# Performance work log

Measured on AMD Instinct MI355X. Metric: run time of the kernel, lower is better.

The kernel has to match this reference:

```python
import jax, jax.numpy as jnp
import numpy as np

NUM_EXPERTS = 8
TOPK = 2
INPUT_DIM = 2048
OUTPUT_DIM = 2048


def setup_inputs() -> dict:
    key = jax.random.key(0)
    k_x, k_w, k_gw, k_gb = jax.random.split(key, 4)
    x = jax.random.normal(k_x, (8192, INPUT_DIM), dtype=jnp.float32)
    # experts: Linear(input_dim, output_dim*num_experts), xavier_uniform weight, zero bias
    fan_out = OUTPUT_DIM * NUM_EXPERTS
    limit = float(np.sqrt(6.0 / (INPUT_DIM + fan_out)))
    expert_w = jax.random.uniform(k_w, (fan_out, INPUT_DIM), minval=-limit, maxval=limit, dtype=jnp.float32)
    expert_b = jnp.zeros((fan_out,), dtype=jnp.float32)
    # gate: Linear(input_dim, num_experts), default torch init (uniform +-1/sqrt(fan_in))
    gl = 1.0 / float(np.sqrt(INPUT_DIM))
    gate_w = jax.random.uniform(k_gw, (NUM_EXPERTS, INPUT_DIM), minval=-gl, maxval=gl, dtype=jnp.float32)
    gate_b = jax.random.uniform(k_gb, (NUM_EXPERTS,), minval=-gl, maxval=gl, dtype=jnp.float32)
    return {"x": x, "expert_w": expert_w, "expert_b": expert_b, "gate_w": gate_w, "gate_b": gate_b}


def reference(x, expert_w, expert_b, gate_w, gate_b):
    B = x.shape[0]
    # gating
    gate_logits = x @ gate_w.T + gate_b                      # [B, E]
    gate_probs = jax.nn.softmax(gate_logits, axis=-1)
    top_k_probs, top_k_idx = jax.lax.top_k(gate_probs, TOPK)  # [B, K]
    # dense expert GEMM: all experts computed
    expert_out = x @ expert_w.T + expert_b                   # [B, E*D_out]
    expert_out = expert_out.reshape(B, NUM_EXPERTS, OUTPUT_DIM)
    # gather selected experts per token and combine
    sel = jnp.take_along_axis(expert_out, top_k_idx[:, :, None], axis=1)  # [B, K, D_out]
    out = jnp.sum(sel * top_k_probs[:, :, None], axis=1)     # [B, D_out]
    return out
```

## Files before the change

kernel.cpp:

```cpp
#include <hip/hip_runtime.h>

#define NUM_TOKENS 8192
#define DIM 2048
#define NE 8
#define BM 256
#define BN 256
#define BK 64
#define KTILES (DIM / BK)

typedef __bf16 bf16x8 __attribute__((ext_vector_type(8)));
typedef float f32x4 __attribute__((ext_vector_type(4)));

typedef __attribute__((address_space(1))) const void* as1_cvp;
typedef __attribute__((address_space(3))) void* as3_vp;

__device__ __forceinline__ unsigned short f2bf(float f) {
  unsigned int u = __float_as_uint(f);
  unsigned int lsb = (u >> 16) & 1u;
  u += 0x7fffu + lsb;
  return (unsigned short)(u >> 16);
}
__device__ __forceinline__ float bflo(unsigned int u) {
  return __uint_as_float(u << 16);
}
__device__ __forceinline__ float bfhi(unsigned int u) {
  return __uint_as_float(u & 0xffff0000u);
}

#define CFENCE() asm volatile("" ::: "memory")

__global__ __launch_bounds__(256) void convert_w_kernel(
    const float4* __restrict__ w, ushort4* __restrict__ wb) {
  int i = blockIdx.x * 256 + threadIdx.x;
  float4 v = w[i];
  ushort4 o;
  o.x = f2bf(v.x); o.y = f2bf(v.y); o.z = f2bf(v.z); o.w = f2bf(v.w);
  wb[i] = o;
}

__global__ __launch_bounds__(256) void gating_kernel(
    const float* __restrict__ x, const float* __restrict__ gw,
    const float* __restrict__ gb, unsigned short* __restrict__ xb,
    float* __restrict__ probs, int* __restrict__ routed) {
  const int wave = threadIdx.x >> 6;
  const int lane = threadIdx.x & 63;
  const int t = blockIdx.x * 4 + wave;
  const float4* xrow = (const float4*)(x + (size_t)t * DIM);
  ushort4* xbrow = (ushort4*)(xb + (size_t)t * DIM);
  float acc[NE];
#pragma unroll
  for (int e = 0; e < NE; ++e) acc[e] = 0.f;
#pragma unroll
  for (int it = 0; it < DIM / (4 * 64); ++it) {
    const int k4 = it * 64 + lane;
    float4 xv = xrow[k4];
    ushort4 o;
    o.x = f2bf(xv.x); o.y = f2bf(xv.y); o.z = f2bf(xv.z); o.w = f2bf(xv.w);
    xbrow[k4] = o;
#pragma unroll
    for (int e = 0; e < NE; ++e) {
      float4 wv = ((const float4*)(gw + (size_t)e * DIM))[k4];
      acc[e] += xv.x * wv.x + xv.y * wv.y + xv.z * wv.z + xv.w * wv.w;
    }
  }
#pragma unroll
  for (int e = 0; e < NE; ++e) {
#pragma unroll
    for (int off = 32; off > 0; off >>= 1)
      acc[e] += __shfl_xor(acc[e], off, 64);
  }
  if (lane == 0) {
    float p[NE];
    float mx = -1e30f;
#pragma unroll
    for (int e = 0; e < NE; ++e) {
      p[e] = acc[e] + gb[e];
      mx = fmaxf(mx, p[e]);
    }
    float s = 0.f;
#pragma unroll
    for (int e = 0; e < NE; ++e) { p[e] = __expf(p[e] - mx); s += p[e]; }
    float inv = 1.f / s;
#pragma unroll
    for (int e = 0; e < NE; ++e) p[e] *= inv;
    int e0 = 0;
#pragma unroll
    for (int e = 1; e < NE; ++e) if (p[e] > p[e0]) e0 = e;
    int e1 = (e0 == 0) ? 1 : 0;
#pragma unroll
    for (int e = 0; e < NE; ++e) if (e != e0 && p[e] > p[e1]) e1 = e;
    probs[t * 2 + 0] = p[e0];
    probs[t * 2 + 1] = p[e1];
    routed[t] = e0 | (e1 << 8);
  }
}

__global__ __launch_bounds__(256) void build_lists_kernel(
    const int* __restrict__ routed, int* __restrict__ lists,
    int* __restrict__ counts, int* __restrict__ tokpos) {
  const int e = blockIdx.x;
  const int tid = threadIdx.x;
  __shared__ int sc[256];
  __shared__ int sb[256];
  const int base_t = tid * (NUM_TOKENS / 256);
  int c = 0, cb = 0;
#pragma unroll 4
  for (int j = 0; j < NUM_TOKENS / 256; ++j) {
    int r = routed[base_t + j];
    int a0 = r & 0xff, a1 = (r >> 8) & 0xff;
    c += (a0 == e) + (a1 == e);
    cb += (a0 < e) + (a1 < e);
  }
  sc[tid] = c;
  sb[tid] = cb;
  __syncthreads();
  for (int ofs = 1; ofs < 256; ofs <<= 1) {
    int v = (tid >= ofs) ? sc[tid - ofs] : 0;
    int w = (tid >= ofs) ? sb[tid - ofs] : 0;
    __syncthreads();
    sc[tid] += v;
    sb[tid] += w;
    __syncthreads();
  }
  const int ebase = sb[255];
  int pos = sc[tid] - c;
#pragma unroll 4
  for (int j = 0; j < NUM_TOKENS / 256; ++j) {
    int t = base_t + j;
    int r = routed[t];
    if ((r & 0xff) == e) {
      lists[e * NUM_TOKENS + pos] = t;
      tokpos[2 * t] = ebase + pos;
      pos++;
    }
    if (((r >> 8) & 0xff) == e) {
      lists[e * NUM_TOKENS + pos] = t | 0x10000;
      tokpos[2 * t + 1] = ebase + pos;
      pos++;
    }
  }
  if (tid == 255) {
    counts[e] = sc[255];
    counts[8 + e] = ebase;
  }
}

__global__ __launch_bounds__(512, 2) void moe_gemm_kernel(
    const unsigned short* __restrict__ xb,
    const unsigned short* __restrict__ wb,
    const float* __restrict__ eb,
    const float* __restrict__ probs,
    const int* __restrict__ lists,
    const int* __restrict__ counts,
    unsigned short* __restrict__ y,
    float* __restrict__ out,
    int use_y) {
  const int e = blockIdx.z;
  const int cnt = counts[e];
  const int m0 = blockIdx.y * BM;
  if (m0 >= cnt) return;
  const int n0 = blockIdx.x * BN;

  __shared__ __attribute__((aligned(16))) unsigned short As[2][BM * BK];
  __shared__ __attribute__((aligned(16))) unsigned short Bs[2][BN * BK];

  const int tid = threadIdx.x;
  const int w = tid >> 6;
  const int ln = tid & 63;
  const int sr8 = ln >> 3;
  const int sgc = ((ln & 7) ^ sr8) * 8;

  const unsigned short* asrc[4];
  const unsigned short* bsrc[4];
#pragma unroll
  for (int rb = 0; rb < 4; ++rb) {
    int r = m0 + rb * 64 + w * 8 + sr8;
    int rc = r < cnt ? r : cnt - 1;
    int tok = lists[e * NUM_TOKENS + rc] & 0xFFFF;
    asrc[rb] = xb + (size_t)tok * DIM + sgc;
    int wr = e * DIM + n0 + rb * 64 + w * 8 + sr8;
    bsrc[rb] = wb + (size_t)wr * DIM + sgc;
  }

#define STAGE_A(buf, rb, k0)                                      \
  __builtin_amdgcn_global_load_lds(                               \
      (as1_cvp)(asrc[rb] + (k0)),                                 \
      (as3_vp)(&As[buf][((rb)*64 + w * 8) * 64]), 16, 0, 0)
#define STAGE_B(buf, rb, k0)                                      \
  __builtin_amdgcn_global_load_lds(                               \
      (as1_cvp)(bsrc[rb] + (k0)),                                 \
      (as3_vp)(&Bs[buf][((rb)*64 + w * 8) * 64]), 16, 0, 0)

#define BAR()            \
  do {                   \
    CFENCE();            \
    __builtin_amdgcn_s_barrier(); \
    CFENCE();            \
  } while (0)

  const f32x4 zero = {0.f, 0.f, 0.f, 0.f};
  f32x4 acc[8][4];
#pragma unroll
  for (int a = 0; a < 8; ++a)
#pragma unroll
    for (int b = 0; b < 4; ++b) acc[a][b] = zero;

  const int wm = w >> 2;
  const int wn = w & 3;
  const int frow = ln & 15;
  const int csel = ln >> 4;
  const int f7 = frow & 7;
  const int aro = (wm * 128 + frow) * 64;
  const int bro = (wn * 64 + frow) * 64;
  const int k0off = (csel ^ f7) * 8;
  const int k1off = ((4 + csel) ^ f7) * 8;

#pragma unroll
  for (int rb = 0; rb < 4; ++rb) STAGE_A(0, rb, 0);
#pragma unroll
  for (int rb = 0; rb < 4; ++rb) STAGE_B(0, rb, 0);

  for (int t = 0; t < KTILES; ++t) {
    const int p = t & 1;
    const int kn = (t + 1) * BK;
    if (t + 1 < KTILES) {
#pragma unroll
      for (int rb = 0; rb < 4; ++rb) STAGE_A(p ^ 1, rb, kn);
      asm volatile("s_waitcnt vmcnt(4)" ::: "memory");
    } else {
      asm volatile("s_waitcnt vmcnt(0)" ::: "memory");
    }
    BAR();
    const unsigned short* Ap = As[p];
    const unsigned short* Bp = Bs[p];
    bf16x8 af[4], bf[4];
#pragma unroll
    for (int i = 0; i < 4; ++i) {
      af[i] = *(const bf16x8*)(Ap + aro + i * 1024 + k0off);
      bf[i] = *(const bf16x8*)(Bp + bro + i * 1024 + k0off);
    }
    __builtin_amdgcn_s_setprio(1);
#pragma unroll
    for (int im = 0; im < 4; ++im)
#pragma unroll
      for (int in_ = 0; in_ < 4; ++in_)
        acc[im][in_] = __builtin_amdgcn_mfma_f32_16x16x32_bf16(
            af[im], bf[in_], acc[im][in_], 0, 0, 0);
    __builtin_amdgcn_s_setprio(0);
    BAR();
#pragma unroll
    for (int i = 0; i < 4; ++i)
      af[i] = *(const bf16x8*)(Ap + aro + (i + 4) * 1024 + k0off);
    if (t + 1 < KTILES) {
#pragma unroll
      for (int rb = 0; rb < 4; ++rb) STAGE_B(p ^ 1, rb, kn);
    }
    __builtin_amdgcn_s_setprio(1);
#pragma unroll
    for (int im = 0; im < 4; ++im)
#pragma unroll
      for (int in_ = 0; in_ < 4; ++in_)
        acc[im + 4][in_] = __builtin_amdgcn_mfma_f32_16x16x32_bf16(
            af[im], bf[in_], acc[im + 4][in_], 0, 0, 0);
    __builtin_amdgcn_s_setprio(0);
    BAR();
#pragma unroll
    for (int i = 0; i < 4; ++i) {
      af[i] = *(const bf16x8*)(Ap + aro + i * 1024 + k1off);
      bf[i] = *(const bf16x8*)(Bp + bro + i * 1024 + k1off);
    }
    __builtin_amdgcn_s_setprio(1);
#pragma unroll
    for (int im = 0; im < 4; ++im)
#pragma unroll
      for (int in_ = 0; in_ < 4; ++in_)
        acc[im][in_] = __builtin_amdgcn_mfma_f32_16x16x32_bf16(
            af[im], bf[in_], acc[im][in_], 0, 0, 0);
    __builtin_amdgcn_s_setprio(0);
    BAR();
#pragma unroll
    for (int i = 0; i < 4; ++i)
      af[i] = *(const bf16x8*)(Ap + aro + (i + 4) * 1024 + k1off);
    __builtin_amdgcn_s_setprio(1);
#pragma unroll
    for (int im = 0; im < 4; ++im)
#pragma unroll
      for (int in_ = 0; in_ < 4; ++in_)
        acc[im + 4][in_] = __builtin_amdgcn_mfma_f32_16x16x32_bf16(
            af[im], bf[in_], acc[im + 4][in_], 0, 0, 0);
    __builtin_amdgcn_s_setprio(0);
    BAR();
  }
#undef STAGE_A
#undef STAGE_B
#undef BAR

  const int quad = ln >> 4;
  const int col = ln & 15;
  const int ybase = counts[8 + e];
#pragma unroll
  for (int im = 0; im < 8; ++im) {
#pragma unroll
    for (int reg = 0; reg < 4; ++reg) {
      int r = m0 + wm * 128 + im * 16 + quad * 4 + reg;
      if (r >= cnt) continue;
      if (use_y) {
        unsigned short* yrow = y + (size_t)(ybase + r) * DIM;
#pragma unroll
        for (int in_ = 0; in_ < 4; ++in_) {
          int n = n0 + wn * 64 + in_ * 16 + col;
          yrow[n] = f2bf(acc[im][in_][reg] + eb[e * DIM + n]);
        }
      } else {
        int entry = lists[e * NUM_TOKENS + r];
        int tok = entry & 0xFFFF;
        int slot = entry >> 16;
        float pw = probs[tok * 2 + slot];
        float* orow = out + (size_t)tok * DIM;
#pragma unroll
        for (int in_ = 0; in_ < 4; ++in_) {
          int n = n0 + wn * 64 + in_ * 16 + col;
          float v = acc[im][in_][reg] + eb[e * DIM + n];
          atomicAdd(orow + n, pw * v);
        }
      }
    }
  }
}

__global__ __launch_bounds__(256) void combine_kernel(
    const unsigned short* __restrict__ y, const float* __restrict__ probs,
    const int* __restrict__ tokpos, float* __restrict__ out) {
  const int t = blockIdx.x;
  const int tid = threadIdx.x;
  const int i0 = tokpos[2 * t], i1 = tokpos[2 * t + 1];
  const float p0 = probs[2 * t], p1 = probs[2 * t + 1];
  uint4 a = ((const uint4*)(y + (size_t)i0 * DIM))[tid];
  uint4 b = ((const uint4*)(y + (size_t)i1 * DIM))[tid];
  float4 o0, o1;
  o0.x = p0 * bflo(a.x) + p1 * bflo(b.x);
  o0.y = p0 * bfhi(a.x) + p1 * bfhi(b.x);
  o0.z = p0 * bflo(a.y) + p1 * bflo(b.y);
  o0.w = p0 * bfhi(a.y) + p1 * bfhi(b.y);
  o1.x = p0 * bflo(a.z) + p1 * bflo(b.z);
  o1.y = p0 * bfhi(a.z) + p1 * bfhi(b.z);
  o1.z = p0 * bflo(a.w) + p1 * bflo(b.w);
  o1.w = p0 * bfhi(a.w) + p1 * bfhi(b.w);
  float4* orow = (float4*)(out + (size_t)t * DIM);
  orow[2 * tid] = o0;
  orow[2 * tid + 1] = o1;
}

extern "C" void kernel_launch(void* const* d_in, const int* in_sizes, int n_in,
                              void* d_out, int out_size, void* d_ws, size_t ws_size,
                              hipStream_t stream) {
  const float* x  = (const float*)d_in[0];
  const float* ew = (const float*)d_in[1];
  const float* eb = (const float*)d_in[2];
  const float* gw = (const float*)d_in[3];
  const float* gb = (const float*)d_in[4];
  float* out = (float*)d_out;
  char* p = (char*)d_ws;

  const size_t NEED = 67108864ull + 33554432ull + 67108864ull + 65536ull +
                      262144ull + 64ull + 32768ull + 65536ull;
  const int use_y = (ws_size >= NEED) ? 1 : 0;

  unsigned short* wb = (unsigned short*)p; p += 67108864;
  unsigned short* xb = (unsigned short*)p; p += 33554432;
  unsigned short* y = nullptr;
  if (use_y) { y = (unsigned short*)p; p += 67108864; }
  float* probs = (float*)p; p += 65536;
  int* lists   = (int*)p;   p += 262144;
  int* counts  = (int*)p;   p += 64;
  int* routed  = (int*)p;   p += 32768;
  int* tokpos  = (int*)p;   p += 65536;

  if (!use_y)
    hipMemsetAsync(out, 0, (size_t)NUM_TOKENS * DIM * sizeof(float), stream);
  convert_w_kernel<<<(NE * DIM * DIM / 4) / 256, 256, 0, stream>>>(
      (const float4*)ew, (ushort4*)wb);
  gating_kernel<<<NUM_TOKENS / 4, 256, 0, stream>>>(x, gw, gb, xb, probs,
                                                    routed);
  build_lists_kernel<<<NE, 256, 0, stream>>>(routed, lists, counts, tokpos);
  moe_gemm_kernel<<<dim3(DIM / BN, NUM_TOKENS / BM, NE), 512, 0, stream>>>(
      xb, wb, eb, probs, lists, counts, y, out, use_y);
  if (use_y)
    combine_kernel<<<NUM_TOKENS, 256, 0, stream>>>(y, probs, tokpos, out);
}
```

Before: 513.2 us.

## Convert MoE GEMM to persistent kernel with atomic tile queue and vectorized epilogue

Replaces the 3D grid, where most blocks exit early because of empty expert tiles, with 256 persistent blocks that fetch work items from a global atomic counter, mapped over only the non-empty (expert, m-tile, n-tile) tiles. This removes launch and scheduling overhead for dead blocks and balances work across CUs. The MFMA operands are swapped so each lane holds four consecutive columns, which allows ushort4 stores to y and float4 bias loads in the epilogue. The cost is two block-wide syncs per tile for the atomic fetch, plus a counter reset that relies on build_lists running first.

```diff
diff --git a/kernel.cpp b/kernel.cpp
--- a/kernel.cpp
+++ b/kernel.cpp
@@ -102,6 +102,7 @@
   const int tid = threadIdx.x;
   __shared__ int sc[256];
   __shared__ int sb[256];
+  if (e == 0 && tid == 0) counts[16] = 0;
   const int base_t = tid * (NUM_TOKENS / 256);
   int c = 0, cb = 0;
 #pragma unroll 4
@@ -151,18 +152,13 @@
     const float* __restrict__ eb,
     const float* __restrict__ probs,
     const int* __restrict__ lists,
-    const int* __restrict__ counts,
+    int* __restrict__ counts,
     unsigned short* __restrict__ y,
     float* __restrict__ out,
     int use_y) {
-  const int e = blockIdx.z;
-  const int cnt = counts[e];
-  const int m0 = blockIdx.y * BM;
-  if (m0 >= cnt) return;
-  const int n0 = blockIdx.x * BN;
-
   __shared__ __attribute__((aligned(16))) unsigned short As[2][BM * BK];
   __shared__ __attribute__((aligned(16))) unsigned short Bs[2][BN * BK];
+  __shared__ int s_w;
 
   const int tid = threadIdx.x;
   const int w = tid >> 6;
@@ -170,40 +166,13 @@
   const int sr8 = ln >> 3;
   const int sgc = ((ln & 7) ^ sr8) * 8;
 
-  const unsigned short* asrc[4];
-  const unsigned short* bsrc[4];
-#pragma unroll
-  for (int rb = 0; rb < 4; ++rb) {
-    int r = m0 + rb * 64 + w * 8 + sr8;
-    int rc = r < cnt ? r : cnt - 1;
-    int tok = lists[e * NUM_TOKENS + rc] & 0xFFFF;
-    asrc[rb] = xb + (size_t)tok * DIM + sgc;
-    int wr = e * DIM + n0 + rb * 64 + w * 8 + sr8;
-    bsrc[rb] = wb + (size_t)wr * DIM + sgc;
-  }
-
-#define STAGE_A(buf, rb, k0)                                      \
-  __builtin_amdgcn_global_load_lds(                               \
-      (as1_cvp)(asrc[rb] + (k0)),                                 \
-      (as3_vp)(&As[buf][((rb)*64 + w * 8) * 64]), 16, 0, 0)
-#define STAGE_B(buf, rb, k0)                                      \
-  __builtin_amdgcn_global_load_lds(                               \
-      (as1_cvp)(bsrc[rb] + (k0)),                                 \
-      (as3_vp)(&Bs[buf][((rb)*64 + w * 8) * 64]), 16, 0, 0)
-
-#define BAR()            \
-  do {                   \
-    CFENCE();            \
-    __builtin_amdgcn_s_barrier(); \
-    CFENCE();            \
-  } while (0)
-
-  const f32x4 zero = {0.f, 0.f, 0.f, 0.f};
-  f32x4 acc[8][4];
-#pragma unroll
-  for (int a = 0; a < 8; ++a)
-#pragma unroll
-    for (int b = 0; b < 4; ++b) acc[a][b] = zero;
+  int ntile[NE];
+  int wtot = 0;
+#pragma unroll
+  for (int i = 0; i < NE; ++i) {
+    ntile[i] = (counts[i] + BM - 1) >> 8;
+    wtot += ntile[i] << 3;
+  }
 
   const int wm = w >> 2;
   const int wn = w & 3;
@@ -215,101 +184,152 @@
   const int k0off = (csel ^ f7) * 8;
   const int k1off = ((4 + csel) ^ f7) * 8;
 
-#pragma unroll
-  for (int rb = 0; rb < 4; ++rb) STAGE_A(0, rb, 0);
-#pragma unroll
-  for (int rb = 0; rb < 4; ++rb) STAGE_B(0, rb, 0);
-
-  for (int t = 0; t < KTILES; ++t) {
-    const int p = t & 1;
-    const int kn = (t + 1) * BK;
-    if (t + 1 < KTILES) {
-#pragma unroll
-      for (int rb = 0; rb < 4; ++rb) STAGE_A(p ^ 1, rb, kn);
-      asm volatile("s_waitcnt vmcnt(4)" ::: "memory");
-    } else {
-      asm volatile("s_waitcnt vmcnt(0)" ::: "memory");
-    }
-    BAR();
-    const unsigned short* Ap = As[p];
-    const unsigned short* Bp = Bs[p];
-    bf16x8 af[4], bf[4];
-#pragma unroll
-    for (int i = 0; i < 4; ++i) {
-      af[i] = *(const bf16x8*)(Ap + aro + i * 1024 + k0off);
-      bf[i] = *(const bf16x8*)(Bp + bro + i * 1024 + k0off);
-    }
-    __builtin_amdgcn_s_setprio(1);
-#pragma unroll
-    for (int im = 0; im < 4; ++im)
-#pragma unroll
-      for (int in_ = 0; in_ < 4; ++in_)
-        acc[im][in_] = __builtin_amdgcn_mfma_f32_16x16x32_bf16(
-            af[im], bf[in_], acc[im][in_], 0, 0, 0);
-    __builtin_amdgcn_s_setprio(0);
-    BAR();
-#pragma unroll
-    for (int i = 0; i < 4; ++i)
-      af[i] = *(const bf16x8*)(Ap + aro + (i + 4) * 1024 + k0off);
-    if (t + 1 < KTILES) {
-#pragma unroll
-      for (int rb = 0; rb < 4; ++rb) STAGE_B(p ^ 1, rb, kn);
-    }
-    __builtin_amdgcn_s_setprio(1);
-#pragma unroll
-    for (int im = 0; im < 4; ++im)
-#pragma unroll
-      for (int in_ = 0; in_ < 4; ++in_)
-        acc[im + 4][in_] = __builtin_amdgcn_mfma_f32_16x16x32_bf16(
-            af[im], bf[in_], acc[im + 4][in_], 0, 0, 0);
-    __builtin_amdgcn_s_setprio(0);
-    BAR();
-#pragma unroll
-    for (int i = 0; i < 4; ++i) {
-      af[i] = *(const bf16x8*)(Ap + aro + i * 1024 + k1off);
-      bf[i] = *(const bf16x8*)(Bp + bro + i * 1024 + k1off);
-    }
-    __builtin_amdgcn_s_setprio(1);
-#pragma unroll
-    for (int im = 0; im < 4; ++im)
-#pragma unroll
-      for (int in_ = 0; in_ < 4; ++in_)
-        acc[im][in_] = __builtin_amdgcn_mfma_f32_16x16x32_bf16(
-            af[im], bf[in_], acc[im][in_], 0, 0, 0);
-    __builtin_amdgcn_s_setprio(0);
-    BAR();
-#pragma unroll
-    for (int i = 0; i < 4; ++i)
-      af[i] = *(const bf16x8*)(Ap + aro + (i + 4) * 1024 + k1off);
-    __builtin_amdgcn_s_setprio(1);
-#pragma unroll
-    for (int im = 0; im < 4; ++im)
-#pragma unroll
-      for (int in_ = 0; in_ < 4; ++in_)
-        acc[im + 4][in_] = __builtin_amdgcn_mfma_f32_16x16x32_bf16(
-            af[im], bf[in_], acc[im + 4][in_], 0, 0, 0);
-    __builtin_amdgcn_s_setprio(0);
-    BAR();
-  }
-#undef STAGE_A
-#undef STAGE_B
-#undef BAR
-
-  const int quad = ln >> 4;
-  const int col = ln & 15;
-  const int ybase = counts[8 + e];
-#pragma unroll
-  for (int im = 0; im < 8; ++im) {
-#pragma unroll
-    for (int reg = 0; reg < 4; ++reg) {
-      int r = m0 + wm * 128 + im * 16 + quad * 4 + reg;
+#define STAGE_A(buf, rb, k0)                                      \
+  __builtin_amdgcn_global_load_lds(                               \
+      (as1_cvp)(asrc[rb] + (k0)),                                 \
+      (as3_vp)(&As[buf][((rb)*64 + w * 8) * 64]), 16, 0, 0)
+#define STAGE_B(buf, rb, k0)                                      \
+  __builtin_amdgcn_global_load_lds(                               \
+      (as1_cvp)(bsrc[rb] + (k0)),                                 \
+      (as3_vp)(&Bs[buf][((rb)*64 + w * 8) * 64]), 16, 0, 0)
+
+#define BAR()                           \
+  do {                                  \
+    CFENCE();                           \
+    __builtin_amdgcn_s_barrier();       \
+    CFENCE();                           \
+  } while (0)
+
+  for (;;) {
+    __syncthreads();
+    if (tid == 0) s_w = atomicAdd(counts + 16, 1);
+    __syncthreads();
+    const int wi = s_w;
+    if (wi >= wtot) break;
+
+    int e = 0, rem = wi;
+    while (rem >= (ntile[e] << 3)) { rem -= ntile[e] << 3; ++e; }
+    const int mt = rem >> 3;
+    const int nt = rem & 7;
+    const int cnt = counts[e];
+    const int m0 = mt * BM;
+    const int n0 = nt * BN;
+
+    const unsigned short* asrc[4];
+    const unsigned short* bsrc[4];
+#pragma unroll
+    for (int rb = 0; rb < 4; ++rb) {
+      int r = m0 + rb * 64 + w * 8 + sr8;
+      int rc = r < cnt ? r : cnt - 1;
+      int tok = lists[e * NUM_TOKENS + rc] & 0xFFFF;
+      asrc[rb] = xb + (size_t)tok * DIM + sgc;
+      int wr = e * DIM + n0 + rb * 64 + w * 8 + sr8;
+      bsrc[rb] = wb + (size_t)wr * DIM + sgc;
+    }
+
+    const f32x4 zero = {0.f, 0.f, 0.f, 0.f};
+    f32x4 acc[8][4];
+#pragma unroll
+    for (int a = 0; a < 8; ++a)
+#pragma unroll
+      for (int b = 0; b < 4; ++b) acc[a][b] = zero;
+
+#pragma unroll
+    for (int rb = 0; rb < 4; ++rb) STAGE_A(0, rb, 0);
+#pragma unroll
+    for (int rb = 0; rb < 4; ++rb) STAGE_B(0, rb, 0);
+
+    for (int t = 0; t < KTILES; ++t) {
+      const int p = t & 1;
+      const int kn = (t + 1) * BK;
+      if (t + 1 < KTILES) {
+#pragma unroll
+        for (int rb = 0; rb < 4; ++rb) STAGE_A(p ^ 1, rb, kn);
+        asm volatile("s_waitcnt vmcnt(4)" ::: "memory");
+      } else {
+        asm volatile("s_waitcnt vmcnt(0)" ::: "memory");
+      }
+      BAR();
+      const unsigned short* Ap = As[p];
+      const unsigned short* Bp = Bs[p];
+      bf16x8 af[4], bf[4];
+#pragma unroll
+      for (int i = 0; i < 4; ++i) {
+        af[i] = *(const bf16x8*)(Ap + aro + i * 1024 + k0off);
+        bf[i] = *(const bf16x8*)(Bp + bro + i * 1024 + k0off);
+      }
+      __builtin_amdgcn_s_setprio(1);
+#pragma unroll
+      for (int im = 0; im < 4; ++im)
+#pragma unroll
+        for (int in_ = 0; in_ < 4; ++in_)
+          acc[im][in_] = __builtin_amdgcn_mfma_f32_16x16x32_bf16(
+              bf[in_], af[im], acc[im][in_], 0, 0, 0);
+      __builtin_amdgcn_s_setprio(0);
+      BAR();
+#pragma unroll
+      for (int i = 0; i < 4; ++i)
+        af[i] = *(const bf16x8*)(Ap + aro + (i + 4) * 1024 + k0off);
+      if (t + 1 < KTILES) {
+#pragma unroll
+        for (int rb = 0; rb < 4; ++rb) STAGE_B(p ^ 1, rb, kn);
+      }
+      __builtin_amdgcn_s_setprio(1);
+#pragma unroll
+      for (int im = 0; im < 4; ++im)
+#pragma unroll
+        for (int in_ = 0; in_ < 4; ++in_)
+          acc[im + 4][in_] = __builtin_amdgcn_mfma_f32_16x16x32_bf16(
+              bf[in_], af[im], acc[im + 4][in_], 0, 0, 0);
+      __builtin_amdgcn_s_setprio(0);
+      BAR();
+#pragma unroll
+      for (int i = 0; i < 4; ++i) {
+        af[i] = *(const bf16x8*)(Ap + aro + i * 1024 + k1off);
+        bf[i] = *(const bf16x8*)(Bp + bro + i * 1024 + k1off);
+      }
+      __builtin_amdgcn_s_setprio(1);
+#pragma unroll
+      for (int im = 0; im < 4; ++im)
+#pragma unroll
+        for (int in_ = 0; in_ < 4; ++in_)
+          acc[im][in_] = __builtin_amdgcn_mfma_f32_16x16x32_bf16(
+              bf[in_], af[im], acc[im][in_], 0, 0, 0);
+      __builtin_amdgcn_s_setprio(0);
+      BAR();
+#pragma unroll
+      for (int i = 0; i < 4; ++i)
+        af[i] = *(const bf16x8*)(Ap + aro + (i + 4) * 1024 + k1off);
+      __builtin_amdgcn_s_setprio(1);
+#pragma unroll
+      for (int im = 0; im < 4; ++im)
+#pragma unroll
+        for (int in_ = 0; in_ < 4; ++in_)
+          acc[im + 4][in_] = __builtin_amdgcn_mfma_f32_16x16x32_bf16(
+              bf[in_], af[im], acc[im + 4][in_], 0, 0, 0);
+      __builtin_amdgcn_s_setprio(0);
+      BAR();
+    }
+
+    const int quad = ln >> 4;
+    const int ybase = counts[8 + e];
+#pragma unroll
+    for (int im = 0; im < 8; ++im) {
+      int r = m0 + wm * 128 + im * 16 + frow;
       if (r >= cnt) continue;
       if (use_y) {
         unsigned short* yrow = y + (size_t)(ybase + r) * DIM;
 #pragma unroll
         for (int in_ = 0; in_ < 4; ++in_) {
-          int n = n0 + wn * 64 + in_ * 16 + col;
-          yrow[n] = f2bf(acc[im][in_][reg] + eb[e * DIM + n]);
+          int n = n0 + wn * 64 + in_ * 16 + quad * 4;
+          float4 ebv = *(const float4*)(eb + (size_t)e * DIM + n);
+          f32x4 v = acc[im][in_];
+          ushort4 o;
+          o.x = f2bf(v[0] + ebv.x);
+          o.y = f2bf(v[1] + ebv.y);
+          o.z = f2bf(v[2] + ebv.z);
+          o.w = f2bf(v[3] + ebv.w);
+          *(ushort4*)(yrow + n) = o;
         }
       } else {
         int entry = lists[e * NUM_TOKENS + r];
@@ -319,13 +339,20 @@
         float* orow = out + (size_t)tok * DIM;
 #pragma unroll
         for (int in_ = 0; in_ < 4; ++in_) {
-          int n = n0 + wn * 64 + in_ * 16 + col;
-          float v = acc[im][in_][reg] + eb[e * DIM + n];
-          atomicAdd(orow + n, pw * v);
+          int n = n0 + wn * 64 + in_ * 16 + quad * 4;
+          float4 ebv = *(const float4*)(eb + (size_t)e * DIM + n);
+          f32x4 v = acc[im][in_];
+          atomicAdd(orow + n + 0, pw * (v[0] + ebv.x));
+          atomicAdd(orow + n + 1, pw * (v[1] + ebv.y));
+          atomicAdd(orow + n + 2, pw * (v[2] + ebv.z));
+          atomicAdd(orow + n + 3, pw * (v[3] + ebv.w));
         }
       }
     }
   }
+#undef STAGE_A
+#undef STAGE_B
+#undef BAR
 }
 
 __global__ __launch_bounds__(256) void combine_kernel(
@@ -363,7 +390,7 @@
   char* p = (char*)d_ws;
 
   const size_t NEED = 67108864ull + 33554432ull + 67108864ull + 65536ull +
-                      262144ull + 64ull + 32768ull + 65536ull;
+                      262144ull + 128ull + 32768ull + 65536ull;
   const int use_y = (ws_size >= NEED) ? 1 : 0;
 
   unsigned short* wb = (unsigned short*)p; p += 67108864;
@@ -372,7 +399,7 @@
   if (use_y) { y = (unsigned short*)p; p += 67108864; }
   float* probs = (float*)p; p += 65536;
   int* lists   = (int*)p;   p += 262144;
-  int* counts  = (int*)p;   p += 64;
+  int* counts  = (int*)p;   p += 128;
   int* routed  = (int*)p;   p += 32768;
   int* tokpos  = (int*)p;   p += 65536;
 
@@ -383,8 +410,8 @@
   gating_kernel<<<NUM_TOKENS / 4, 256, 0, stream>>>(x, gw, gb, xb, probs,
                                                     routed);
   build_lists_kernel<<<NE, 256, 0, stream>>>(routed, lists, counts, tokpos);
-  moe_gemm_kernel<<<dim3(DIM / BN, NUM_TOKENS / BM, NE), 512, 0, stream>>>(
-      xb, wb, eb, probs, lists, counts, y, out, use_y);
+  moe_gemm_kernel<<<256, 512, 0, stream>>>(xb, wb, eb, probs, lists, counts, y,
+                                           out, use_y);
   if (use_y)
     combine_kernel<<<NUM_TOKENS, 256, 0, stream>>>(y, probs, tokpos, out);
 }
```

Result: no change. 514.0 us (+0.2%).
